# Kernel optimization log

Measured on AMD Instinct MI355X. Metric: run time of the kernel, lower is better.

Reference implementation:

```python
import jax, jax.numpy as jnp
import numpy as np

MARGIN = 0.5
ALPHA = 0.5
BATCH_SZ = 8192
K = 20
B = 8192
C = 5000
N_RARE = 50
D_EMB = 64


def _minority_classes(tnp, batch_sz):
    # faithful numpy port of get_minority_classes (structure only, on host)
    counts = tnp.sum(0)
    order = np.argsort(counts, kind='stable')
    sc = counts[order]
    m = np.cumsum(sc) <= 0.5 * batch_sz
    kept_ix = order[m]
    kept_counts = sc[m]
    srt = np.argsort(kept_ix, kind='stable')
    sorted_classes = kept_ix[srt]
    return sorted_classes[kept_counts[srt] > 1]


def _crl_sums(preds_min, y_min_np, k):
    # Per minority class: hard-mine k lowest-scored positives (excluding the
    # anchor itself) and, per the original code's indexing, the k lowest-scored
    # negative *predictions* (neg_preds[:k] despite neg_idxs[-k:] -- kept faithful).
    # Triplet rows are the cartesian product anchor x pos x neg, and TripletLoss
    # uses reduction='sum', so the loss only needs the global sums of |a-p| and
    # |a-n| over all triplet rows.
    dp = jnp.float32(0.0)
    dn = jnp.float32(0.0)
    has_anchor = False
    for j in range(y_min_np.shape[1]):
        pos_rows = np.nonzero(y_min_np[:, j] == 1)[0]
        c_p = pos_rows.size
        if c_p == 0:
            continue
        has_anchor = True
        neg_rows = np.nonzero(y_min_np[:, j] != 1)[0]
        pp = preds_min[pos_rows, j]            # [c_p] anchor/positive preds
        np_a = min(k, c_p - 1)                 # positives mined per anchor
        n_n = min(k, neg_rows.size)            # negatives mined per class
        xs = jnp.sort(pp)
        ranks = jnp.argsort(jnp.argsort(pp))   # rank of each anchor in xs
        # selected sorted positions for anchor with rank r:
        #   {j <= np_a, j != r} if r <= np_a else {j < np_a}
        limit = jnp.where(ranks <= np_a, np_a + 1, np_a)
        Jix = jnp.arange(c_p)
        M = (Jix[None, :] < limit[:, None]) & (Jix[None, :] != ranks[:, None])
        pos_sum = jnp.sum(jnp.where(M, jnp.abs(pp[:, None] - xs[None, :]), 0.0))
        dp = dp + jnp.float32(n_n) * pos_sum   # each pos pair repeats n_n times
        if n_n > 0:
            neg_sel = jnp.sort(preds_min[neg_rows, j])[:n_n]
            neg_sum = jnp.sum(jnp.abs(pp[:, None] - neg_sel[None, :]))
            dn = dn + jnp.float32(np_a) * neg_sum  # each neg repeats np_a times
    return dp, dn, has_anchor


def _bce_with_logits(logits, target):
    # numerically stable BCEWithLogitsLoss (mean reduction)
    return jnp.mean(jnp.maximum(logits, 0.0) - logits * target
                    + jnp.log1p(jnp.exp(-jnp.abs(logits))))


def _forward(logits, target, tnp):
    bce = _bce_with_logits(logits, target)
    idxs = _minority_classes(tnp, BATCH_SZ)
    preds = jax.nn.sigmoid(logits)
    preds_min = preds[:, idxs]                 # [B, n_minority]
    y_min_np = tnp[:, idxs]
    dp, dn, has_anchor = _crl_sums(preds_min, y_min_np, K)
    if not has_anchor:
        return bce                             # torch.cat([]) RuntimeError path
    crl = jax.nn.relu(dp - dn + MARGIN)
    return ALPHA * crl + (1.0 - ALPHA) * bce


def setup_inputs() -> dict:
    key = jax.random.key(0)
    k1, k2, k3 = jax.random.split(key, 3)
    logits = jax.random.normal(k1, (B, C), dtype=jnp.float32)
    # 50 rare classes (p=0.003) -> minority set; rest frequent (p=0.5)
    p = jnp.where(jnp.arange(C) < N_RARE, 0.003, 0.5)
    target = (jax.random.uniform(k2, (B, C)) < p[None, :]).astype(jnp.float32)
    X = jax.random.normal(k3, (B, D_EMB), dtype=jnp.float32)
    return {"input": logits, "target": target, "X": X}


def reference(input, target, X):
    tnp = np.asarray(target)  # structural (index) computation on host
    return _forward(input, target, tnp)
```

## Files before the change

### kernel.cpp

```cpp
#include <hip/hip_runtime.h>
#include <math.h>

#define BB 8192
#define CC 5000
#define KTOP 20
#define MAXP 4096
#define MARGIN 0.5
#define ALPHA 0.5

#define WS_ACC(ws)    ((double*)(ws))
#define WS_NMIN(ws)   ((int*)((char*)(ws) + 24))
#define WS_COUNTS(ws) ((int*)((char*)(ws) + 32))
#define WS_FLAGS(ws)  ((int*)((char*)(ws) + 32 + CC*4))
#define WS_MINOR(ws)  ((int*)((char*)(ws) + 32 + 2*CC*4))

__global__ void init_kernel(double* acc, int* nmin, int* counts) {
    int gid = blockIdx.x * blockDim.x + threadIdx.x;
    if (gid == 0) { acc[0] = 0.0; acc[1] = 0.0; acc[2] = 0.0; *nmin = 0; }
    for (int i = gid; i < CC; i += gridDim.x * blockDim.x) counts[i] = 0;
}

__device__ __forceinline__ float bce_term_fast(float l, float t) {
    float e = __expf(-fabsf(l));
    float sp = __logf(1.0f + e);
    return fmaxf(l, 0.0f) - l * t + sp;
}

__global__ __launch_bounds__(256)
void bce_counts_kernel(const float* __restrict__ logits, const float* __restrict__ target,
                       double* __restrict__ acc, int* __restrict__ counts) {
    int tid = threadIdx.x;
    int c4 = blockIdx.x * 256 + tid;
    int r0 = blockIdx.y * 32;
    float bce = 0.0f;
    int cnt0 = 0, cnt1 = 0, cnt2 = 0, cnt3 = 0;
    if (c4 < 1250) {
        const float4* L = (const float4*)logits;
        const float4* T = (const float4*)target;
        for (int r = r0; r < r0 + 32; ++r) {
            float4 l = L[(size_t)r * 1250 + c4];
            float4 t = T[(size_t)r * 1250 + c4];
            bce += bce_term_fast(l.x, t.x) + bce_term_fast(l.y, t.y)
                 + bce_term_fast(l.z, t.z) + bce_term_fast(l.w, t.w);
            cnt0 += (t.x == 1.0f); cnt1 += (t.y == 1.0f);
            cnt2 += (t.z == 1.0f); cnt3 += (t.w == 1.0f);
        }
        int c = c4 * 4;
        if (cnt0) atomicAdd(&counts[c + 0], cnt0);
        if (cnt1) atomicAdd(&counts[c + 1], cnt1);
        if (cnt2) atomicAdd(&counts[c + 2], cnt2);
        if (cnt3) atomicAdd(&counts[c + 3], cnt3);
    }
    __shared__ double sd[256];
    sd[tid] = (double)bce;
    __syncthreads();
    for (int s = 128; s > 0; s >>= 1) {
        if (tid < s) sd[tid] += sd[tid + s];
        __syncthreads();
    }
    if (tid == 0) atomicAdd(&acc[0], sd[0]);
}

__global__ __launch_bounds__(256)
void minority_flag_kernel(const int* __restrict__ counts, int* __restrict__ flags) {
    __shared__ int sc[CC];
    int tid = threadIdx.x;
    for (int i = tid; i < CC; i += 256) sc[i] = counts[i];
    __syncthreads();
    int wave = tid >> 6;
    int lane = tid & 63;
    int j = blockIdx.x * 4 + wave;
    if (j >= CC) return;
    int cj = sc[j];
    int flag = 0;
    if (cj > 1) {
        int cum = 0;
        for (int k = lane; k < CC; k += 64) {
            int ck = sc[k];
            if (ck < cj || (ck == cj && k <= j)) cum += ck;
        }
        for (int off = 32; off > 0; off >>= 1) cum += __shfl_down(cum, off);
        flag = (cum <= (BB / 2));
    }
    if (lane == 0) flags[j] = flag;
}

__global__ __launch_bounds__(256)
void compact_kernel(const int* __restrict__ flags, int* __restrict__ minor,
                    int* __restrict__ nmin) {
    const int CH = 20;
    int tid = threadIdx.x;
    int f[CH];
    int c = 0;
    #pragma unroll
    for (int i = 0; i < CH; ++i) {
        int j = tid * CH + i;
        int v = (j < CC) ? flags[j] : 0;
        f[i] = v; c += v;
    }
    __shared__ int ssum[256];
    ssum[tid] = c;
    __syncthreads();
    for (int off = 1; off < 256; off <<= 1) {
        int v = ssum[tid];
        int add = (tid >= off) ? ssum[tid - off] : 0;
        __syncthreads();
        ssum[tid] = v + add;
        __syncthreads();
    }
    int pos = ssum[tid] - c;
    #pragma unroll
    for (int i = 0; i < CH; ++i) {
        if (f[i]) minor[pos++] = tid * CH + i;
    }
    if (tid == 255) *nmin = ssum[255];
}

__global__ __launch_bounds__(256)
void crl_kernel(const float* __restrict__ logits, const float* __restrict__ target,
                const int* __restrict__ minor, const int* __restrict__ nmin,
                double* __restrict__ acc) {
    __shared__ float pos[MAXP];
    __shared__ float neglist[256 * KTOP];
    __shared__ float negwave[4 * KTOP];
    __shared__ float negsel[KTOP];
    __shared__ double sd[256];
    __shared__ int pcount;
    int tid = threadIdx.x;
    int lane = tid & 63;
    int wave = tid >> 6;
    int nm = *nmin;

    for (int m = blockIdx.x; m < nm; m += gridDim.x) {
        int j = minor[m];
        if (tid == 0) pcount = 0;
        for (int i = 0; i < KTOP; ++i) neglist[tid * KTOP + i] = INFINITY;
        __syncthreads();

        const float* tcol = target + j;
        const float* xcol = logits + j;
        float tv[32], xv[32];
        #pragma unroll
        for (int i = 0; i < 32; ++i) {
            size_t r = (size_t)(tid + i * 256);
            tv[i] = tcol[r * CC];
            xv[i] = xcol[r * CC];
        }
        #pragma unroll
        for (int i = 0; i < 32; ++i) {
            float x = xv[i];
            float e = __expf(-fabsf(x));
            float inv = __builtin_amdgcn_rcpf(1.0f + e);
            float s = (x >= 0.0f) ? inv : e * inv;
            if (tv[i] == 1.0f) {
                int slot = atomicAdd(&pcount, 1);
                if (slot < MAXP) pos[slot] = s;
            } else {
                float* lst = &neglist[tid * KTOP];
                if (s < lst[KTOP - 1]) {
                    int p = KTOP - 1;
                    while (p > 0 && lst[p - 1] > s) { lst[p] = lst[p - 1]; --p; }
                    lst[p] = s;
                }
            }
        }
        __syncthreads();
        int cp = min(pcount, MAXP);

        int n = 1;
        while (n < cp) n <<= 1;
        for (int i = cp + tid; i < n; i += 256) pos[i] = INFINITY;
        __syncthreads();
        for (int k = 2; k <= n; k <<= 1) {
            for (int jj = k >> 1; jj > 0; jj >>= 1) {
                for (int i = tid; i < n; i += 256) {
                    int ixj = i ^ jj;
                    if (ixj > i) {
                        float a = pos[i], b = pos[ixj];
                        bool up = ((i & k) == 0);
                        if (up ? (a > b) : (a < b)) { pos[i] = b; pos[ixj] = a; }
                    }
                }
                __syncthreads();
            }
        }

        {
            int head = 0;
            for (int round = 0; round < KTOP; ++round) {
                float v = (head < KTOP) ? neglist[tid * KTOP + head] : INFINITY;
                int idx = lane;
                for (int off = 32; off > 0; off >>= 1) {
                    float ov = __shfl_xor(v, off);
                    int oi = __shfl_xor(idx, off);
                    if (ov < v || (ov == v && oi < idx)) { v = ov; idx = oi; }
                }
                if (lane == 0) negwave[wave * KTOP + round] = v;
                if (lane == idx) head++;
            }
        }
        __syncthreads();
        if (tid == 0) {
            int h0 = 0, h1 = 0, h2 = 0, h3 = 0;
            for (int r = 0; r < KTOP; ++r) {
                float v0 = (h0 < KTOP) ? negwave[0 * KTOP + h0] : INFINITY;
                float v1 = (h1 < KTOP) ? negwave[1 * KTOP + h1] : INFINITY;
                float v2 = (h2 < KTOP) ? negwave[2 * KTOP + h2] : INFINITY;
                float v3 = (h3 < KTOP) ? negwave[3 * KTOP + h3] : INFINITY;
                float best = v0; int bi = 0;
                if (v1 < best) { best = v1; bi = 1; }
                if (v2 < best) { best = v2; bi = 2; }
                if (v3 < best) { best = v3; bi = 3; }
                negsel[r] = best;
                if (bi == 0) h0++; else if (bi == 1) h1++; else if (bi == 2) h2++; else h3++;
            }
        }
        __syncthreads();

        int np_a = min(KTOP, cp - 1);
        int n_n = min(KTOP, BB - cp);

        double lsum = 0.0;
        for (int r = tid; r < cp; r += 256) {
            float v = pos[r];
            int L = (r <= np_a) ? np_a : np_a - 1;
            double s = 0.0;
            for (int l = 0; l <= L; ++l) s += (double)fabsf(v - pos[l]);
            lsum += s;
        }
        sd[tid] = lsum;
        __syncthreads();
        for (int s = 128; s > 0; s >>= 1) {
            if (tid < s) sd[tid] += sd[tid + s];
            __syncthreads();
        }
        double pos_sum = sd[0];
        __syncthreads();

        lsum = 0.0;
        for (int r = tid; r < cp; r += 256) {
            float v = pos[r];
            double s = 0.0;
            for (int l = 0; l < n_n; ++l) s += (double)fabsf(v - negsel[l]);
            lsum += s;
        }
        sd[tid] = lsum;
        __syncthreads();
        for (int s = 128; s > 0; s >>= 1) {
            if (tid < s) sd[tid] += sd[tid + s];
            __syncthreads();
        }
        if (tid == 0) {
            atomicAdd(&acc[1], (double)n_n * pos_sum);
            atomicAdd(&acc[2], (double)np_a * sd[0]);
        }
        __syncthreads();
    }
}

__global__ void finalize_kernel(const double* __restrict__ acc, const int* __restrict__ nmin,
                                float* __restrict__ out) {
    if (blockIdx.x == 0 && threadIdx.x == 0) {
        double bce = acc[0] / ((double)BB * (double)CC);
        double result;
        if (*nmin > 0) {
            double crl = acc[1] - acc[2] + MARGIN;
            if (crl < 0.0) crl = 0.0;
            result = ALPHA * crl + (1.0 - ALPHA) * bce;
        } else {
            result = bce;
        }
        out[0] = (float)result;
    }
}

extern "C" void kernel_launch(void* const* d_in, const int* in_sizes, int n_in,
                              void* d_out, int out_size, void* d_ws, size_t ws_size,
                              hipStream_t stream) {
    const float* logits = (const float*)d_in[0];
    const float* target = (const float*)d_in[1];
    float* out = (float*)d_out;

    double* acc  = WS_ACC(d_ws);
    int* nmin    = WS_NMIN(d_ws);
    int* counts  = WS_COUNTS(d_ws);
    int* flags   = WS_FLAGS(d_ws);
    int* minor   = WS_MINOR(d_ws);

    init_kernel<<<20, 256, 0, stream>>>(acc, nmin, counts);
    bce_counts_kernel<<<dim3(5, 256), 256, 0, stream>>>(logits, target, acc, counts);
    minority_flag_kernel<<<1250, 256, 0, stream>>>(counts, flags);
    compact_kernel<<<1, 256, 0, stream>>>(flags, minor, nmin);
    crl_kernel<<<64, 256, 0, stream>>>(logits, target, minor, nmin, acc);
    finalize_kernel<<<1, 64, 0, stream>>>(acc, nmin, out);
}
```

Before: 439.8 us.

## Split CRL gather across row blocks and reduce in a separate kernel

The single per-class CRL kernel, where one block read all 8192 rows of a column, is split in two. A gather kernel spreads each minority column over 16 row blocks. Each block appends positive predictions into a global buffer whose per-class offsets come from a prefix sum over class counts, and writes its local top-20 negatives. A reduce kernel then bitonic-sorts the positives and the merged 320 negative candidates per class. This raises parallelism for the strided column reads, at the cost of an extra launch, global atomics and intermediate buffers.

```diff
diff --git a/kernel.cpp b/kernel.cpp
--- a/kernel.cpp
+++ b/kernel.cpp
@@ -4,20 +4,27 @@
 #define BB 8192
 #define CC 5000
 #define KTOP 20
-#define MAXP 4096
 #define MARGIN 0.5
 #define ALPHA 0.5
+#define NM_MAX 2048
+#define NRB 16
+#define RPB 512
 
 #define WS_ACC(ws)    ((double*)(ws))
 #define WS_NMIN(ws)   ((int*)((char*)(ws) + 24))
 #define WS_COUNTS(ws) ((int*)((char*)(ws) + 32))
-#define WS_FLAGS(ws)  ((int*)((char*)(ws) + 32 + CC*4))
-#define WS_MINOR(ws)  ((int*)((char*)(ws) + 32 + 2*CC*4))
-
-__global__ void init_kernel(double* acc, int* nmin, int* counts) {
+#define WS_FLAGS(ws)  ((int*)((char*)(ws) + 20032))
+#define WS_MINOR(ws)  ((int*)((char*)(ws) + 40032))
+#define WS_POSOFF(ws) ((int*)((char*)(ws) + 48224))
+#define WS_PCNT(ws)   ((int*)((char*)(ws) + 56424))
+#define WS_POSBUF(ws) ((float*)((char*)(ws) + 64616))
+#define WS_NEGBLK(ws) ((float*)((char*)(ws) + 81256))
+
+__global__ void init_kernel(double* acc, int* nmin, int* counts, int* pcnt) {
     int gid = blockIdx.x * blockDim.x + threadIdx.x;
     if (gid == 0) { acc[0] = 0.0; acc[1] = 0.0; acc[2] = 0.0; *nmin = 0; }
     for (int i = gid; i < CC; i += gridDim.x * blockDim.x) counts[i] = 0;
+    for (int i = gid; i < NM_MAX; i += gridDim.x * blockDim.x) pcnt[i] = 0;
 }
 
 __device__ __forceinline__ float bce_term_fast(float l, float t) {
@@ -86,10 +93,15 @@
 }
 
 __global__ __launch_bounds__(256)
-void compact_kernel(const int* __restrict__ flags, int* __restrict__ minor,
-                    int* __restrict__ nmin) {
+void compact_kernel(const int* __restrict__ flags, const int* __restrict__ counts,
+                    int* __restrict__ minor, int* __restrict__ nmin,
+                    int* __restrict__ posoff) {
     const int CH = 20;
     int tid = threadIdx.x;
+    __shared__ int ssum[256];
+    __shared__ int sminor[NM_MAX];
+    __shared__ int snm;
+
     int f[CH];
     int c = 0;
     #pragma unroll
@@ -98,7 +110,6 @@
         int v = (j < CC) ? flags[j] : 0;
         f[i] = v; c += v;
     }
-    __shared__ int ssum[256];
     ssum[tid] = c;
     __syncthreads();
     for (int off = 1; off < 256; off <<= 1) {
@@ -111,66 +122,154 @@
     int pos = ssum[tid] - c;
     #pragma unroll
     for (int i = 0; i < CH; ++i) {
-        if (f[i]) minor[pos++] = tid * CH + i;
-    }
-    if (tid == 255) *nmin = ssum[255];
-}
-
-__global__ __launch_bounds__(256)
-void crl_kernel(const float* __restrict__ logits, const float* __restrict__ target,
-                const int* __restrict__ minor, const int* __restrict__ nmin,
-                double* __restrict__ acc) {
-    __shared__ float pos[MAXP];
-    __shared__ float neglist[256 * KTOP];
-    __shared__ float negwave[4 * KTOP];
-    __shared__ float negsel[KTOP];
-    __shared__ double sd[256];
-    __shared__ int pcount;
+        if (f[i]) { sminor[pos] = tid * CH + i; minor[pos] = tid * CH + i; pos++; }
+    }
+    if (tid == 255) { snm = ssum[255]; *nmin = snm; }
+    __syncthreads();
+    int nm = snm;
+
+    const int CH2 = NM_MAX / 256;
+    int cc2[CH2];
+    int c2 = 0;
+    #pragma unroll
+    for (int i = 0; i < CH2; ++i) {
+        int idx = tid * CH2 + i;
+        int v = (idx < nm) ? counts[sminor[idx]] : 0;
+        cc2[i] = v; c2 += v;
+    }
+    __syncthreads();
+    ssum[tid] = c2;
+    __syncthreads();
+    for (int off = 1; off < 256; off <<= 1) {
+        int v = ssum[tid];
+        int add = (tid >= off) ? ssum[tid - off] : 0;
+        __syncthreads();
+        ssum[tid] = v + add;
+        __syncthreads();
+    }
+    int p2 = ssum[tid] - c2;
+    #pragma unroll
+    for (int i = 0; i < CH2; ++i) {
+        int idx = tid * CH2 + i;
+        if (idx < nm) posoff[idx] = p2;
+        p2 += cc2[i];
+    }
+    if (tid == 255) posoff[nm] = ssum[255];
+}
+
+__global__ __launch_bounds__(256)
+void crl_gather_kernel(const float* __restrict__ logits, const float* __restrict__ target,
+                       const int* __restrict__ minor, const int* __restrict__ nmin,
+                       const int* __restrict__ posoff, int* __restrict__ pcnt,
+                       float* __restrict__ posbuf, float* __restrict__ negblk) {
+    __shared__ float negwv[4 * KTOP];
     int tid = threadIdx.x;
     int lane = tid & 63;
     int wave = tid >> 6;
     int nm = *nmin;
+    int gy = blockIdx.y;
 
     for (int m = blockIdx.x; m < nm; m += gridDim.x) {
         int j = minor[m];
-        if (tid == 0) pcount = 0;
-        for (int i = 0; i < KTOP; ++i) neglist[tid * KTOP + i] = INFINITY;
-        __syncthreads();
-
-        const float* tcol = target + j;
-        const float* xcol = logits + j;
-        float tv[32], xv[32];
-        #pragma unroll
-        for (int i = 0; i < 32; ++i) {
-            size_t r = (size_t)(tid + i * 256);
-            tv[i] = tcol[r * CC];
-            xv[i] = xcol[r * CC];
-        }
-        #pragma unroll
-        for (int i = 0; i < 32; ++i) {
-            float x = xv[i];
-            float e = __expf(-fabsf(x));
-            float inv = __builtin_amdgcn_rcpf(1.0f + e);
-            float s = (x >= 0.0f) ? inv : e * inv;
-            if (tv[i] == 1.0f) {
-                int slot = atomicAdd(&pcount, 1);
-                if (slot < MAXP) pos[slot] = s;
-            } else {
-                float* lst = &neglist[tid * KTOP];
-                if (s < lst[KTOP - 1]) {
-                    int p = KTOP - 1;
-                    while (p > 0 && lst[p - 1] > s) { lst[p] = lst[p - 1]; --p; }
-                    lst[p] = s;
-                }
+        size_t rA = (size_t)gy * RPB + tid;
+        size_t rB = rA + 256;
+        float tA = target[rA * CC + j];
+        float xA = logits[rA * CC + j];
+        float tB = target[rB * CC + j];
+        float xB = logits[rB * CC + j];
+
+        float eA = __expf(-fabsf(xA));
+        float iA = __builtin_amdgcn_rcpf(1.0f + eA);
+        float sA = (xA >= 0.0f) ? iA : eA * iA;
+        float eB = __expf(-fabsf(xB));
+        float iB = __builtin_amdgcn_rcpf(1.0f + eB);
+        float sB = (xB >= 0.0f) ? iB : eB * iB;
+
+        int off = posoff[m];
+        int cap = posoff[m + 1] - off;
+        float v0, v1;
+        if (tA == 1.0f) {
+            int slot = atomicAdd(&pcnt[m], 1);
+            if (slot < cap) posbuf[off + slot] = sA;
+            v0 = INFINITY;
+        } else v0 = sA;
+        if (tB == 1.0f) {
+            int slot = atomicAdd(&pcnt[m], 1);
+            if (slot < cap) posbuf[off + slot] = sB;
+            v1 = INFINITY;
+        } else v1 = sB;
+        if (v1 < v0) { float tmp = v0; v0 = v1; v1 = tmp; }
+
+        int h = 0;
+        for (int round = 0; round < KTOP; ++round) {
+            float v = (h == 0) ? v0 : ((h == 1) ? v1 : INFINITY);
+            int idx = lane;
+            for (int o = 32; o > 0; o >>= 1) {
+                float ov = __shfl_xor(v, o);
+                int oi = __shfl_xor(idx, o);
+                if (ov < v || (ov == v && oi < idx)) { v = ov; idx = oi; }
             }
-        }
-        __syncthreads();
-        int cp = min(pcount, MAXP);
+            if (lane == 0) negwv[wave * KTOP + round] = v;
+            if (lane == idx) h++;
+        }
+        __syncthreads();
+        if (tid == 0) {
+            int h0 = 0, h1 = 0, h2 = 0, h3 = 0;
+            float* dst = &negblk[((size_t)m * NRB + gy) * KTOP];
+            for (int r = 0; r < KTOP; ++r) {
+                float a0 = (h0 < KTOP) ? negwv[0 * KTOP + h0] : INFINITY;
+                float a1 = (h1 < KTOP) ? negwv[1 * KTOP + h1] : INFINITY;
+                float a2 = (h2 < KTOP) ? negwv[2 * KTOP + h2] : INFINITY;
+                float a3 = (h3 < KTOP) ? negwv[3 * KTOP + h3] : INFINITY;
+                float best = a0; int bi = 0;
+                if (a1 < best) { best = a1; bi = 1; }
+                if (a2 < best) { best = a2; bi = 2; }
+                if (a3 < best) { best = a3; bi = 3; }
+                dst[r] = best;
+                if (bi == 0) h0++; else if (bi == 1) h1++; else if (bi == 2) h2++; else h3++;
+            }
+        }
+        __syncthreads();
+    }
+}
+
+__global__ __launch_bounds__(256)
+void crl_reduce_kernel(const int* __restrict__ nmin, const int* __restrict__ posoff,
+                       const float* __restrict__ posbuf, const float* __restrict__ negblk,
+                       double* __restrict__ acc) {
+    __shared__ float pos[4096];
+    __shared__ float neg[512];
+    __shared__ float negsel[KTOP];
+    __shared__ double sd[256];
+    int tid = threadIdx.x;
+    int nm = *nmin;
+
+    for (int m = blockIdx.x; m < nm; m += gridDim.x) {
+        int off = posoff[m];
+        int cp = posoff[m + 1] - off;
 
         int n = 1;
         while (n < cp) n <<= 1;
-        for (int i = cp + tid; i < n; i += 256) pos[i] = INFINITY;
-        __syncthreads();
+        for (int i = tid; i < n; i += 256) pos[i] = (i < cp) ? posbuf[off + i] : INFINITY;
+        const float* src = &negblk[(size_t)m * NRB * KTOP];
+        for (int i = tid; i < 512; i += 256) neg[i] = (i < NRB * KTOP) ? src[i] : INFINITY;
+        __syncthreads();
+
+        for (int k = 2; k <= 512; k <<= 1) {
+            for (int jj = k >> 1; jj > 0; jj >>= 1) {
+                for (int i = tid; i < 512; i += 256) {
+                    int ixj = i ^ jj;
+                    if (ixj > i) {
+                        float a = neg[i], b = neg[ixj];
+                        bool up = ((i & k) == 0);
+                        if (up ? (a > b) : (a < b)) { neg[i] = b; neg[ixj] = a; }
+                    }
+                }
+                __syncthreads();
+            }
+        }
+        if (tid < KTOP) negsel[tid] = neg[tid];
+
         for (int k = 2; k <= n; k <<= 1) {
             for (int jj = k >> 1; jj > 0; jj >>= 1) {
                 for (int i = tid; i < n; i += 256) {
@@ -185,38 +284,6 @@
             }
         }
 
-        {
-            int head = 0;
-            for (int round = 0; round < KTOP; ++round) {
-                float v = (head < KTOP) ? neglist[tid * KTOP + head] : INFINITY;
-                int idx = lane;
-                for (int off = 32; off > 0; off >>= 1) {
-                    float ov = __shfl_xor(v, off);
-                    int oi = __shfl_xor(idx, off);
-                    if (ov < v || (ov == v && oi < idx)) { v = ov; idx = oi; }
-                }
-                if (lane == 0) negwave[wave * KTOP + round] = v;
-                if (lane == idx) head++;
-            }
-        }
-        __syncthreads();
-        if (tid == 0) {
-            int h0 = 0, h1 = 0, h2 = 0, h3 = 0;
-            for (int r = 0; r < KTOP; ++r) {
-                float v0 = (h0 < KTOP) ? negwave[0 * KTOP + h0] : INFINITY;
-                float v1 = (h1 < KTOP) ? negwave[1 * KTOP + h1] : INFINITY;
-                float v2 = (h2 < KTOP) ? negwave[2 * KTOP + h2] : INFINITY;
-                float v3 = (h3 < KTOP) ? negwave[3 * KTOP + h3] : INFINITY;
-                float best = v0; int bi = 0;
-                if (v1 < best) { best = v1; bi = 1; }
-                if (v2 < best) { best = v2; bi = 2; }
-                if (v3 < best) { best = v3; bi = 3; }
-                negsel[r] = best;
-                if (bi == 0) h0++; else if (bi == 1) h1++; else if (bi == 2) h2++; else h3++;
-            }
-        }
-        __syncthreads();
-
         int np_a = min(KTOP, cp - 1);
         int n_n = min(KTOP, BB - cp);
 
@@ -286,11 +353,17 @@
     int* counts  = WS_COUNTS(d_ws);
     int* flags   = WS_FLAGS(d_ws);
     int* minor   = WS_MINOR(d_ws);
-
-    init_kernel<<<20, 256, 0, stream>>>(acc, nmin, counts);
+    int* posoff  = WS_POSOFF(d_ws);
+    int* pcnt    = WS_PCNT(d_ws);
+    float* posbuf = WS_POSBUF(d_ws);
+    float* negblk = WS_NEGBLK(d_ws);
+
+    init_kernel<<<20, 256, 0, stream>>>(acc, nmin, counts, pcnt);
     bce_counts_kernel<<<dim3(5, 256), 256, 0, stream>>>(logits, target, acc, counts);
     minority_flag_kernel<<<1250, 256, 0, stream>>>(counts, flags);
-    compact_kernel<<<1, 256, 0, stream>>>(flags, minor, nmin);
-    crl_kernel<<<64, 256, 0, stream>>>(logits, target, minor, nmin, acc);
+    compact_kernel<<<1, 256, 0, stream>>>(flags, counts, minor, nmin, posoff);
+    crl_gather_kernel<<<dim3(64, NRB), 256, 0, stream>>>(logits, target, minor, nmin,
+                                                         posoff, pcnt, posbuf, negblk);
+    crl_reduce_kernel<<<64, 256, 0, stream>>>(nmin, posoff, posbuf, negblk, acc);
     finalize_kernel<<<1, 64, 0, stream>>>(acc, nmin, out);
 }
```

New measurement: 407.5 us. 1.08x faster.

## Drop compaction kernel, launch CRL per class, register-resident negative top-k

Applied to the files above, without the earlier changes.

Removes the single-block compaction kernel. The flag kernel now counts minority classes atomically, and the CRL kernel launches one block per class that exits early when the class is not flagged, instead of 64 persistent blocks looping over the compacted list. The per-thread negative top-k insertion moves from LDS into a branchless register list, and the cross-wave merge is done by one wave. The BCE kernel gets unrolled 4-row batched loads and an occupancy hint. The cost is 5000 mostly-empty block launches, plus more registers per CRL thread.

```diff
diff --git a/kernel.cpp b/kernel.cpp
--- a/kernel.cpp
+++ b/kernel.cpp
@@ -11,8 +11,7 @@
 #define WS_ACC(ws)    ((double*)(ws))
 #define WS_NMIN(ws)   ((int*)((char*)(ws) + 24))
 #define WS_COUNTS(ws) ((int*)((char*)(ws) + 32))
-#define WS_FLAGS(ws)  ((int*)((char*)(ws) + 32 + CC*4))
-#define WS_MINOR(ws)  ((int*)((char*)(ws) + 32 + 2*CC*4))
+#define WS_FLAGS(ws)  ((int*)((char*)(ws) + 20032))
 
 __global__ void init_kernel(double* acc, int* nmin, int* counts) {
     int gid = blockIdx.x * blockDim.x + threadIdx.x;
@@ -26,7 +25,7 @@
     return fmaxf(l, 0.0f) - l * t + sp;
 }
 
-__global__ __launch_bounds__(256)
+__global__ __launch_bounds__(256, 4)
 void bce_counts_kernel(const float* __restrict__ logits, const float* __restrict__ target,
                        double* __restrict__ acc, int* __restrict__ counts) {
     int tid = threadIdx.x;
@@ -35,15 +34,23 @@
     float bce = 0.0f;
     int cnt0 = 0, cnt1 = 0, cnt2 = 0, cnt3 = 0;
     if (c4 < 1250) {
-        const float4* L = (const float4*)logits;
-        const float4* T = (const float4*)target;
-        for (int r = r0; r < r0 + 32; ++r) {
-            float4 l = L[(size_t)r * 1250 + c4];
-            float4 t = T[(size_t)r * 1250 + c4];
-            bce += bce_term_fast(l.x, t.x) + bce_term_fast(l.y, t.y)
-                 + bce_term_fast(l.z, t.z) + bce_term_fast(l.w, t.w);
-            cnt0 += (t.x == 1.0f); cnt1 += (t.y == 1.0f);
-            cnt2 += (t.z == 1.0f); cnt3 += (t.w == 1.0f);
+        const float4* Lb = (const float4*)logits + (size_t)r0 * 1250 + c4;
+        const float4* Tb = (const float4*)target + (size_t)r0 * 1250 + c4;
+        #pragma unroll
+        for (int rb = 0; rb < 32; rb += 4) {
+            float4 lv[4], tv[4];
+            #pragma unroll
+            for (int u = 0; u < 4; ++u) {
+                lv[u] = Lb[(size_t)(rb + u) * 1250];
+                tv[u] = Tb[(size_t)(rb + u) * 1250];
+            }
+            #pragma unroll
+            for (int u = 0; u < 4; ++u) {
+                bce += bce_term_fast(lv[u].x, tv[u].x) + bce_term_fast(lv[u].y, tv[u].y)
+                     + bce_term_fast(lv[u].z, tv[u].z) + bce_term_fast(lv[u].w, tv[u].w);
+                cnt0 += (tv[u].x == 1.0f); cnt1 += (tv[u].y == 1.0f);
+                cnt2 += (tv[u].z == 1.0f); cnt3 += (tv[u].w == 1.0f);
+            }
         }
         int c = c4 * 4;
         if (cnt0) atomicAdd(&counts[c + 0], cnt0);
@@ -62,7 +69,8 @@
 }
 
 __global__ __launch_bounds__(256)
-void minority_flag_kernel(const int* __restrict__ counts, int* __restrict__ flags) {
+void minority_flag_kernel(const int* __restrict__ counts, int* __restrict__ flags,
+                          int* __restrict__ nmin) {
     __shared__ int sc[CC];
     int tid = threadIdx.x;
     for (int i = tid; i < CC; i += 256) sc[i] = counts[i];
@@ -82,179 +90,145 @@
         for (int off = 32; off > 0; off >>= 1) cum += __shfl_down(cum, off);
         flag = (cum <= (BB / 2));
     }
-    if (lane == 0) flags[j] = flag;
-}
-
-__global__ __launch_bounds__(256)
-void compact_kernel(const int* __restrict__ flags, int* __restrict__ minor,
-                    int* __restrict__ nmin) {
-    const int CH = 20;
-    int tid = threadIdx.x;
-    int f[CH];
-    int c = 0;
-    #pragma unroll
-    for (int i = 0; i < CH; ++i) {
-        int j = tid * CH + i;
-        int v = (j < CC) ? flags[j] : 0;
-        f[i] = v; c += v;
-    }
-    __shared__ int ssum[256];
-    ssum[tid] = c;
-    __syncthreads();
-    for (int off = 1; off < 256; off <<= 1) {
-        int v = ssum[tid];
-        int add = (tid >= off) ? ssum[tid - off] : 0;
-        __syncthreads();
-        ssum[tid] = v + add;
-        __syncthreads();
-    }
-    int pos = ssum[tid] - c;
-    #pragma unroll
-    for (int i = 0; i < CH; ++i) {
-        if (f[i]) minor[pos++] = tid * CH + i;
-    }
-    if (tid == 255) *nmin = ssum[255];
-}
-
-__global__ __launch_bounds__(256)
+    if (lane == 0) {
+        flags[j] = flag;
+        if (flag) atomicAdd(nmin, 1);
+    }
+}
+
+__global__ __launch_bounds__(256, 1)
 void crl_kernel(const float* __restrict__ logits, const float* __restrict__ target,
-                const int* __restrict__ minor, const int* __restrict__ nmin,
-                double* __restrict__ acc) {
+                const int* __restrict__ flags, double* __restrict__ acc) {
+    int j = blockIdx.x;
+    if (!flags[j]) return;
+
     __shared__ float pos[MAXP];
-    __shared__ float neglist[256 * KTOP];
-    __shared__ float negwave[4 * KTOP];
+    __shared__ float neg_lds[KTOP * 256];
     __shared__ float negsel[KTOP];
     __shared__ double sd[256];
     __shared__ int pcount;
     int tid = threadIdx.x;
     int lane = tid & 63;
-    int wave = tid >> 6;
-    int nm = *nmin;
-
-    for (int m = blockIdx.x; m < nm; m += gridDim.x) {
-        int j = minor[m];
-        if (tid == 0) pcount = 0;
-        for (int i = 0; i < KTOP; ++i) neglist[tid * KTOP + i] = INFINITY;
+    int wv = tid >> 6;
+
+    if (tid == 0) pcount = 0;
+    __syncthreads();
+
+    float xv[32], tv[32];
+    #pragma unroll
+    for (int i = 0; i < 32; ++i) {
+        size_t r = (size_t)i * 256 + tid;
+        tv[i] = target[r * CC + j];
+        xv[i] = logits[r * CC + j];
+    }
+
+    float lst[KTOP];
+    #pragma unroll
+    for (int k = 0; k < KTOP; ++k) lst[k] = INFINITY;
+    #pragma unroll
+    for (int i = 0; i < 32; ++i) {
+        float x = xv[i];
+        float e = __expf(-fabsf(x));
+        float inv = __builtin_amdgcn_rcpf(1.0f + e);
+        float s = (x >= 0.0f) ? inv : e * inv;
+        bool isp = (tv[i] == 1.0f);
+        if (isp) {
+            int slot = atomicAdd(&pcount, 1);
+            if (slot < MAXP) pos[slot] = s;
+        }
+        float v = isp ? INFINITY : s;
+        #pragma unroll
+        for (int k = KTOP - 1; k >= 1; --k) {
+            lst[k] = (v < lst[k - 1]) ? lst[k - 1] : ((v < lst[k]) ? v : lst[k]);
+        }
+        lst[0] = fminf(lst[0], v);
+    }
+
+    #pragma unroll
+    for (int k = 0; k < KTOP; ++k) neg_lds[k * 256 + tid] = lst[k];
+    __syncthreads();
+
+    if (wv == 0) {
+        int h0 = 0, h1 = 0, h2 = 0, h3 = 0;
+        for (int round = 0; round < KTOP; ++round) {
+            float v0 = (h0 < KTOP) ? neg_lds[h0 * 256 + lane      ] : INFINITY;
+            float v1 = (h1 < KTOP) ? neg_lds[h1 * 256 + lane +  64] : INFINITY;
+            float v2 = (h2 < KTOP) ? neg_lds[h2 * 256 + lane + 128] : INFINITY;
+            float v3 = (h3 < KTOP) ? neg_lds[h3 * 256 + lane + 192] : INFINITY;
+            float vm = fminf(fminf(v0, v1), fminf(v2, v3));
+            float v = vm; int idx = lane;
+            for (int o = 32; o > 0; o >>= 1) {
+                float ov = __shfl_xor(v, o);
+                int oi = __shfl_xor(idx, o);
+                if (ov < v || (ov == v && oi < idx)) { v = ov; idx = oi; }
+            }
+            if (lane == 0) negsel[round] = v;
+            if (lane == idx) {
+                if (vm == v0) h0++;
+                else if (vm == v1) h1++;
+                else if (vm == v2) h2++;
+                else h3++;
+            }
+        }
+    }
+    __syncthreads();
+
+    int cp = min(pcount, MAXP);
+
+    int n = 1;
+    while (n < cp) n <<= 1;
+    for (int i = cp + tid; i < n; i += 256) pos[i] = INFINITY;
+    __syncthreads();
+    for (int k = 2; k <= n; k <<= 1) {
+        for (int jj = k >> 1; jj > 0; jj >>= 1) {
+            for (int i = tid; i < n; i += 256) {
+                int ixj = i ^ jj;
+                if (ixj > i) {
+                    float a = pos[i], b = pos[ixj];
+                    bool up = ((i & k) == 0);
+                    if (up ? (a > b) : (a < b)) { pos[i] = b; pos[ixj] = a; }
+                }
+            }
+            __syncthreads();
+        }
+    }
+
+    int np_a = min(KTOP, cp - 1);
+    int n_n = min(KTOP, BB - cp);
+
+    double lsum = 0.0;
+    for (int r = tid; r < cp; r += 256) {
+        float v = pos[r];
+        int L = (r <= np_a) ? np_a : np_a - 1;
+        double s = 0.0;
+        for (int l = 0; l <= L; ++l) s += (double)fabsf(v - pos[l]);
+        lsum += s;
+    }
+    sd[tid] = lsum;
+    __syncthreads();
+    for (int s = 128; s > 0; s >>= 1) {
+        if (tid < s) sd[tid] += sd[tid + s];
         __syncthreads();
-
-        const float* tcol = target + j;
-        const float* xcol = logits + j;
-        float tv[32], xv[32];
-        #pragma unroll
-        for (int i = 0; i < 32; ++i) {
-            size_t r = (size_t)(tid + i * 256);
-            tv[i] = tcol[r * CC];
-            xv[i] = xcol[r * CC];
-        }
-        #pragma unroll
-        for (int i = 0; i < 32; ++i) {
-            float x = xv[i];
-            float e = __expf(-fabsf(x));
-            float inv = __builtin_amdgcn_rcpf(1.0f + e);
-            float s = (x >= 0.0f) ? inv : e * inv;
-            if (tv[i] == 1.0f) {
-                int slot = atomicAdd(&pcount, 1);
-                if (slot < MAXP) pos[slot] = s;
-            } else {
-                float* lst = &neglist[tid * KTOP];
-                if (s < lst[KTOP - 1]) {
-                    int p = KTOP - 1;
-                    while (p > 0 && lst[p - 1] > s) { lst[p] = lst[p - 1]; --p; }
-                    lst[p] = s;
-                }
-            }
-        }
+    }
+    double pos_sum = sd[0];
+    __syncthreads();
+
+    lsum = 0.0;
+    for (int r = tid; r < cp; r += 256) {
+        float v = pos[r];
+        double s = 0.0;
+        for (int l = 0; l < n_n; ++l) s += (double)fabsf(v - negsel[l]);
+        lsum += s;
+    }
+    sd[tid] = lsum;
+    __syncthreads();
+    for (int s = 128; s > 0; s >>= 1) {
+        if (tid < s) sd[tid] += sd[tid + s];
         __syncthreads();
-        int cp = min(pcount, MAXP);
-
-        int n = 1;
-        while (n < cp) n <<= 1;
-        for (int i = cp + tid; i < n; i += 256) pos[i] = INFINITY;
-        __syncthreads();
-        for (int k = 2; k <= n; k <<= 1) {
-            for (int jj = k >> 1; jj > 0; jj >>= 1) {
-                for (int i = tid; i < n; i += 256) {
-                    int ixj = i ^ jj;
-                    if (ixj > i) {
-                        float a = pos[i], b = pos[ixj];
-                        bool up = ((i & k) == 0);
-                        if (up ? (a > b) : (a < b)) { pos[i] = b; pos[ixj] = a; }
-                    }
-                }
-                __syncthreads();
-            }
-        }
-
-        {
-            int head = 0;
-            for (int round = 0; round < KTOP; ++round) {
-                float v = (head < KTOP) ? neglist[tid * KTOP + head] : INFINITY;
-                int idx = lane;
-                for (int off = 32; off > 0; off >>= 1) {
-                    float ov = __shfl_xor(v, off);
-                    int oi = __shfl_xor(idx, off);
-                    if (ov < v || (ov == v && oi < idx)) { v = ov; idx = oi; }
-                }
-                if (lane == 0) negwave[wave * KTOP + round] = v;
-                if (lane == idx) head++;
-            }
-        }
-        __syncthreads();
-        if (tid == 0) {
-            int h0 = 0, h1 = 0, h2 = 0, h3 = 0;
-            for (int r = 0; r < KTOP; ++r) {
-                float v0 = (h0 < KTOP) ? negwave[0 * KTOP + h0] : INFINITY;
-                float v1 = (h1 < KTOP) ? negwave[1 * KTOP + h1] : INFINITY;
-                float v2 = (h2 < KTOP) ? negwave[2 * KTOP + h2] : INFINITY;
-                float v3 = (h3 < KTOP) ? negwave[3 * KTOP + h3] : INFINITY;
-                float best = v0; int bi = 0;
-                if (v1 < best) { best = v1; bi = 1; }
-                if (v2 < best) { best = v2; bi = 2; }
-                if (v3 < best) { best = v3; bi = 3; }
-                negsel[r] = best;
-                if (bi == 0) h0++; else if (bi == 1) h1++; else if (bi == 2) h2++; else h3++;
-            }
-        }
-        __syncthreads();
-
-        int np_a = min(KTOP, cp - 1);
-        int n_n = min(KTOP, BB - cp);
-
-        double lsum = 0.0;
-        for (int r = tid; r < cp; r += 256) {
-            float v = pos[r];
-            int L = (r <= np_a) ? np_a : np_a - 1;
-            double s = 0.0;
-            for (int l = 0; l <= L; ++l) s += (double)fabsf(v - pos[l]);
-            lsum += s;
-        }
-        sd[tid] = lsum;
-        __syncthreads();
-        for (int s = 128; s > 0; s >>= 1) {
-            if (tid < s) sd[tid] += sd[tid + s];
-            __syncthreads();
-        }
-        double pos_sum = sd[0];
-        __syncthreads();
-
-        lsum = 0.0;
-        for (int r = tid; r < cp; r += 256) {
-            float v = pos[r];
-            double s = 0.0;
-            for (int l = 0; l < n_n; ++l) s += (double)fabsf(v - negsel[l]);
-            lsum += s;
-        }
-        sd[tid] = lsum;
-        __syncthreads();
-        for (int s = 128; s > 0; s >>= 1) {
-            if (tid < s) sd[tid] += sd[tid + s];
-            __syncthreads();
-        }
-        if (tid == 0) {
-            atomicAdd(&acc[1], (double)n_n * pos_sum);
-            atomicAdd(&acc[2], (double)np_a * sd[0]);
-        }
-        __syncthreads();
+    }
+    if (tid == 0) {
+        atomicAdd(&acc[1], (double)n_n * pos_sum);
+        atomicAdd(&acc[2], (double)np_a * sd[0]);
     }
 }
 
@@ -285,12 +259,10 @@
     int* nmin    = WS_NMIN(d_ws);
     int* counts  = WS_COUNTS(d_ws);
     int* flags   = WS_FLAGS(d_ws);
-    int* minor   = WS_MINOR(d_ws);
 
     init_kernel<<<20, 256, 0, stream>>>(acc, nmin, counts);
     bce_counts_kernel<<<dim3(5, 256), 256, 0, stream>>>(logits, target, acc, counts);
-    minority_flag_kernel<<<1250, 256, 0, stream>>>(counts, flags);
-    compact_kernel<<<1, 256, 0, stream>>>(flags, minor, nmin);
-    crl_kernel<<<64, 256, 0, stream>>>(logits, target, minor, nmin, acc);
+    minority_flag_kernel<<<1250, 256, 0, stream>>>(counts, flags, nmin);
+    crl_kernel<<<CC, 256, 0, stream>>>(logits, target, flags, acc);
     finalize_kernel<<<1, 64, 0, stream>>>(acc, nmin, out);
 }
```

After: 564.7 us. 28.4% more time.
